# Kernel optimization log

Hardware: AMD Instinct MI355X
Metric: run time of the kernel (lower is better)

The kernel has to match this reference:

```python
import jax, jax.numpy as jnp
import numpy as np


def setup_inputs() -> dict:
    key = jax.random.key(0)
    ks = jax.random.split(key, 8)
    B, S, H = 2, 2048, 2048
    Hq, Hkv, D = 16, 4, H // 16
    s = 0.02
    return {
        "query": jax.random.normal(ks[0], (B, S, H), jnp.float32),
        "key": jax.random.normal(ks[1], (B, S, H), jnp.float32),
        "value": jax.random.normal(ks[2], (B, S, H), jnp.float32),
        "Wq": jax.random.normal(ks[3], (H, Hq * D), jnp.float32) * s,
        "bq": jnp.zeros((Hq * D,), jnp.float32),
        "Wk": jax.random.normal(ks[4], (H, Hkv * D), jnp.float32) * s,
        "bk": jnp.zeros((Hkv * D,), jnp.float32),
        "Wv": jax.random.normal(ks[5], (H, Hkv * D), jnp.float32) * s,
        "bv": jnp.zeros((Hkv * D,), jnp.float32),
        "Wo": jax.random.normal(ks[6], (H, H), jnp.float32) * s,
        "bo": jnp.zeros((H,), jnp.float32),
    }


def reference(query, key, value, Wq, bq, Wk, bk, Wv, bv, Wo, bo):
    Hq, Hkv = 16, 4
    B, S, H = query.shape
    D = H // Hq
    G = Hq // Hkv  # heads per KV group
    # projections
    q = query @ Wq + bq   # [B,S,Hq*D]
    k = key @ Wk + bk     # [B,S,Hkv*D]
    v = value @ Wv + bv   # [B,S,Hkv*D]
    # [B, Hkv(groups), G(heads per group), S, D] for q; [B, Hkv, S, D] for k,v
    q = q.reshape(B, S, Hkv, G, D).transpose(0, 2, 3, 1, 4)
    k = k.reshape(B, S, Hkv, D).transpose(0, 2, 1, 3)
    v = v.reshape(B, S, Hkv, D).transpose(0, 2, 1, 3)
    # NOTE: original module applies NO 1/sqrt(D) scaling -- kept faithful.
    attn = jnp.einsum('bghqd,bgkd->bghqk', q, k)  # [B,Hkv,G,S,S]
    attn = jax.nn.softmax(attn, axis=-1)
    out = jnp.einsum('bghqk,bgkd->bghqd', attn, v)  # [B,Hkv,G,S,D]
    # permute(0,3,1,2,4) -> [B,S,Hkv,G,D] -> [B,S,H]
    out = out.transpose(0, 3, 1, 2, 4).reshape(B, S, H)
    return out @ Wo + bo
```

## Files before the change

### kernel.cpp

```cpp
#include <hip/hip_runtime.h>
#include <hip/hip_bf16.h>
#include <type_traits>
#include <stdint.h>

typedef short bf16x8 __attribute__((ext_vector_type(8)));
typedef short short4v __attribute__((ext_vector_type(4)));
typedef float f32x4 __attribute__((ext_vector_type(4)));
typedef float f32x16 __attribute__((ext_vector_type(16)));

#define GLL16(gp, lp) __builtin_amdgcn_global_load_lds( \
    (const __attribute__((address_space(1))) void*)(gp), \
    (__attribute__((address_space(3))) void*)(lp), 16, 0, 0)

__device__ inline short f2bf(float f) {
    union { float f; uint32_t u; } v;
    v.f = f;
    uint32_t r = (v.u + 0x7FFFu + ((v.u >> 16) & 1u)) >> 16;
    return (short)(uint16_t)r;
}

__device__ inline bf16x8 cvt8(const float4& a, const float4& b) {
    bf16x8 o;
    o[0] = f2bf(a.x); o[1] = f2bf(a.y); o[2] = f2bf(a.z); o[3] = f2bf(a.w);
    o[4] = f2bf(b.x); o[5] = f2bf(b.y); o[6] = f2bf(b.z); o[7] = f2bf(b.w);
    return o;
}

__device__ inline uint32_t cvtpk(float lo, float hi) {
    uint32_t r;
    asm("v_cvt_pk_bf16_f32 %0, %1, %2" : "=v"(r) : "v"(lo), "v"(hi));
    return r;
}

__device__ inline bf16x8 mk8(uint32_t a, uint32_t b, uint32_t c, uint32_t d) {
    union { uint32_t u[4]; bf16x8 v; } t;
    t.u[0] = a; t.u[1] = b; t.u[2] = c; t.u[3] = d;
    return t.v;
}

__device__ inline void xchg_pf(const uint32_t c[8], bool hib, bf16x8& fA, bf16x8& fB) {
    uint32_t p0 = (uint32_t)__shfl_xor((int)c[0], 32);
    uint32_t p1 = (uint32_t)__shfl_xor((int)c[1], 32);
    uint32_t p2 = (uint32_t)__shfl_xor((int)c[2], 32);
    uint32_t p3 = (uint32_t)__shfl_xor((int)c[3], 32);
    fA = mk8(hib ? p2 : c[0], hib ? p3 : c[1], hib ? c[2] : p0, hib ? c[3] : p1);
    uint32_t p4 = (uint32_t)__shfl_xor((int)c[4], 32);
    uint32_t p5 = (uint32_t)__shfl_xor((int)c[5], 32);
    uint32_t p6 = (uint32_t)__shfl_xor((int)c[6], 32);
    uint32_t p7 = (uint32_t)__shfl_xor((int)c[7], 32);
    fB = mk8(hib ? p6 : c[4], hib ? p7 : c[5], hib ? c[6] : p4, hib ? c[7] : p5);
}

__global__ __launch_bounds__(256) void cvtk(const float* __restrict__ in,
                                            short* __restrict__ out, int n8)
{
    int i = blockIdx.x * blockDim.x + threadIdx.x;
    int stride = gridDim.x * blockDim.x;
    for (; i < n8; i += stride) {
        const float4* p = (const float4*)(in + (size_t)i * 8);
        float4 a = p[0], b = p[1];
        *(bf16x8*)(out + (size_t)i * 8) = cvt8(a, b);
    }
}

__global__ __launch_bounds__(256) void cvt3(
    const float* __restrict__ q, const float* __restrict__ k, const float* __restrict__ v,
    short* __restrict__ Xq, short* __restrict__ Xk, short* __restrict__ Xv)
{
    const float* in; short* out;
    if (blockIdx.y == 0) { in = q; out = Xq; }
    else if (blockIdx.y == 1) { in = k; out = Xk; }
    else { in = v; out = Xv; }
    size_t i = (size_t)blockIdx.x * 256 + threadIdx.x;
    const float4* p = (const float4*)(in + i * 8);
    float4 a = p[0], b = p[1];
    *(bf16x8*)(out + i * 8) = cvt8(a, b);
}

__global__ __launch_bounds__(256) void transW4(
    const float* __restrict__ W0, const float* __restrict__ W1,
    const float* __restrict__ W2, const float* __restrict__ W3,
    short* __restrict__ T0, short* __restrict__ T1,
    short* __restrict__ T2, short* __restrict__ T3)
{
    const int K = 2048;
    const float* W; short* T; int N;
    int z = blockIdx.z;
    if (z == 0)      { W = W0; T = T0; N = 2048; }
    else if (z == 1) { W = W1; T = T1; N = 512; }
    else if (z == 2) { W = W2; T = T2; N = 512; }
    else             { W = W3; T = T3; N = 2048; }
    int n0 = blockIdx.x * 64, k0 = blockIdx.y * 64;
    if (n0 >= N) return;
    __shared__ short Tt[64][65];
    int t = threadIdx.x;
    int kl = t >> 2, nb = (t & 3) * 16;
    const float* wp = W + (size_t)(k0 + kl) * N + n0 + nb;
    #pragma unroll
    for (int j = 0; j < 16; ++j) Tt[nb + j][kl] = f2bf(wp[j]);
    __syncthreads();
    int nl = t >> 2, kb = (t & 3) * 16;
    short* op = T + (size_t)(n0 + nl) * K + k0 + kb;
    #pragma unroll
    for (int j = 0; j < 16; ++j) op[j] = Tt[nl][kb + j];
}

__global__ __launch_bounds__(256) void transV(const short* __restrict__ Vb,
                                              short* __restrict__ Vt)
{
    __shared__ short T[64][65];
    int s0 = blockIdx.x * 64, d0 = blockIdx.y * 64, bg = blockIdx.z;
    int b = bg >> 2, g = bg & 3;
    int t = threadIdx.x;
    int sl = t >> 2, db = (t & 3) * 16;
    const short* vp = Vb + (size_t)(b * 2048 + s0 + sl) * 512 + g * 128 + d0 + db;
    #pragma unroll
    for (int j = 0; j < 16; ++j) T[db + j][sl] = vp[j];
    __syncthreads();
    int dl = t >> 2, sb = (t & 3) * 16;
    short* op = Vt + (size_t)(bg * 128 + d0 + dl) * 2048 + s0 + sb;
    #pragma unroll
    for (int j = 0; j < 16; ++j) op[j] = T[dl][sb + j];
}

template <typename TC>
__device__ __forceinline__ void gemm_core(
    const short* __restrict__ A, const short* __restrict__ BT,
    const float* __restrict__ bias, TC* __restrict__ C,
    int N, int K, int m0, int n0, short* As, short* Bs)
{
    const int t = threadIdx.x, w = t >> 6, lane = t & 63;
    const int lr = lane & 15, lg = lane >> 4;
    const int wm = (w >> 1) * 64, wn = (w & 1) * 64;
    f32x4 acc[4][4] = {};

    const int lrow = lane >> 3;
    const int lcg = (lane & 7) ^ (lrow & 7);
    const int sw = lr & 7;

    const short* abase[2]; const short* bbase[2];
    #pragma unroll
    for (int kc = 0; kc < 2; ++kc) {
        abase[kc] = &As[(wm + lr) * 64 + (((kc * 4 + lg) ^ sw) * 8)];
        bbase[kc] = &Bs[(wn + lr) * 64 + (((kc * 4 + lg) ^ sw) * 8)];
    }
    const short* asrc = A  + (size_t)(m0 + w * 32 + lrow) * K + lcg * 8;
    const short* bsrc = BT + (size_t)(n0 + w * 32 + lrow) * K + lcg * 8;
    short* adst = &As[(w * 32) * 64];
    short* bdst = &Bs[(w * 32) * 64];

    for (int kk = 0; kk < K; kk += 64) {
        __syncthreads();
        #pragma unroll
        for (int i = 0; i < 4; ++i) {
            GLL16(asrc + (size_t)i * 8 * K, adst + i * 512);
            GLL16(bsrc + (size_t)i * 8 * K, bdst + i * 512);
        }
        asrc += 64; bsrc += 64;
        __syncthreads();
        #pragma unroll
        for (int kc = 0; kc < 2; ++kc) {
            bf16x8 af[4], bfr[4];
            #pragma unroll
            for (int i = 0; i < 4; ++i) af[i] = *(const bf16x8*)(abase[kc] + i * 1024);
            #pragma unroll
            for (int j = 0; j < 4; ++j) bfr[j] = *(const bf16x8*)(bbase[kc] + j * 1024);
            #pragma unroll
            for (int i = 0; i < 4; ++i)
                #pragma unroll
                for (int j = 0; j < 4; ++j)
                    acc[i][j] = __builtin_amdgcn_mfma_f32_16x16x32_bf16(af[i], bfr[j], acc[i][j], 0, 0, 0);
        }
    }

    #pragma unroll
    for (int i = 0; i < 4; ++i) {
        #pragma unroll
        for (int j = 0; j < 4; ++j) {
            #pragma unroll
            for (int r = 0; r < 4; ++r) {
                int row = m0 + wm + i * 16 + lg * 4 + r;
                int col = n0 + wn + j * 16 + lr;
                float v = acc[i][j][r] + bias[col];
                if constexpr (std::is_same<TC, short>::value)
                    C[(size_t)row * N + col] = f2bf(v);
                else
                    C[(size_t)row * N + col] = v;
            }
        }
    }
}

template <typename TC>
__global__ __launch_bounds__(256) void gemm_std(
    const short* __restrict__ A, const short* __restrict__ BT,
    const float* __restrict__ bias, TC* __restrict__ C, int N, int K)
{
    __shared__ short As[128 * 64];
    __shared__ short Bs[128 * 64];
    int bid = blockIdx.x;
    int chunk = gridDim.x >> 3;
    int wg = (bid & 7) * chunk + (bid >> 3);
    int m0 = (wg & 31) * 128, n0 = (wg >> 5) * 128;
    gemm_core<TC>(A, BT, bias, C, N, K, m0, n0, As, Bs);
}

__global__ __launch_bounds__(256) void gemm_qkv(
    const short* __restrict__ Xq, const short* __restrict__ Xk, const short* __restrict__ Xv,
    const short* __restrict__ WqT, const short* __restrict__ WkT, const short* __restrict__ WvT,
    const float* __restrict__ bq, const float* __restrict__ bk, const float* __restrict__ bv,
    short* __restrict__ Qb, short* __restrict__ Kb, short* __restrict__ Vb)
{
    __shared__ short As[128 * 64];
    __shared__ short Bs[128 * 64];
    int bid = blockIdx.x;
    int wg = (bid & 7) * 96 + (bid >> 3);
    const short* A; const short* BT; const float* bi; short* C; int N; int l;
    if (wg < 512)      { l = wg;       A = Xq; BT = WqT; bi = bq; C = Qb; N = 2048; }
    else if (wg < 640) { l = wg - 512; A = Xk; BT = WkT; bi = bk; C = Kb; N = 512; }
    else               { l = wg - 640; A = Xv; BT = WvT; bi = bv; C = Vb; N = 512; }
    int m0 = (l & 31) * 128, n0 = (l >> 5) * 128;
    gemm_core<short>(A, BT, bi, C, N, 2048, m0, n0, As, Bs);
}

__global__ __launch_bounds__(256, 2) void attn_kernel(
    const short* __restrict__ Qb, const short* __restrict__ Kb,
    const short* __restrict__ Vt, short* __restrict__ Ob)
{
    const int S = 2048;
    __shared__ short Ks[2 * 64 * 128];
    __shared__ short Vs[2 * 128 * 64];

    int bid = blockIdx.x;
    int wg = (bid & 7) * 64 + (bid >> 3);
    const int qt = wg & 15, bh = wg >> 4;
    const int b = bh >> 4, h = bh & 15, g = h >> 2, bg = b * 4 + g;

    const int t = threadIdx.x, w = t >> 6, lane = t & 63;
    const int l5 = lane & 31, hi = lane >> 5;
    const bool hib = hi != 0;
    const int qg = b * S + qt * 128 + w * 32 + l5;
    const float C = 1.44269504089f;

    const short* qrow = Qb + (size_t)qg * 2048 + h * 128 + hi * 8;
    bf16x8 qf[8];
    #pragma unroll
    for (int dm = 0; dm < 8; ++dm)
        qf[dm] = *(const bf16x8*)(qrow + dm * 16);

    f32x16 o[4] = {};
    float m = -1e30f, l = 0.0f;

    const int sr4 = lane >> 4, sc4 = lane & 15;
    const int sr8 = lane >> 3, sc8 = lane & 7;
    const short* ksrc[4]; const short* vsrc[4];
    #pragma unroll
    for (int i = 0; i < 4; ++i) {
        int kr = w * 16 + i * 4 + sr4;
        ksrc[i] = Kb + (size_t)(b * S + kr) * 512 + g * 128 + ((sc4 ^ (kr & 15)) * 8);
        int d = w * 32 + i * 8 + sr8;
        vsrc[i] = Vt + (size_t)(bg * 128 + d) * 2048 + ((sc8 ^ (d & 7)) * 8);
    }

    int kx[8];
    #pragma unroll
    for (int dm = 0; dm < 8; ++dm)
        kx[dm] = (((dm * 2 + hi) ^ (l5 & 15)) * 8);
    int va[4];
    #pragma unroll
    for (int j = 0; j < 4; ++j)
        va[j] = (((2 * j + hi) ^ (l5 & 7)) * 8);

    #define STAGE(BUF, KVI) do { \
        short* kd = Ks + (BUF) * 8192 + (w * 16) * 128; \
        short* vd = Vs + (BUF) * 8192 + (w * 32) * 64; \
        size_t ko = (size_t)(KVI) * 64 * 512; \
        int vo = (KVI) * 64; \
        _Pragma("unroll") \
        for (int i = 0; i < 4; ++i) { \
            GLL16(ksrc[i] + ko, kd + i * 512); \
            GLL16(vsrc[i] + vo, vd + i * 512); \
        } \
    } while (0)

    STAGE(0, 0);
    const int NT = S / 64;
    for (int ti = 0; ti < NT; ++ti) {
        int cur = ti & 1;
        __syncthreads();
        if (ti + 1 < NT) STAGE(cur ^ 1, ti + 1);

        const short* KB = Ks + cur * 8192 + l5 * 128;
        f32x16 p0 = {}, p1 = {};
        #pragma unroll
        for (int dm = 0; dm < 8; ++dm) {
            bf16x8 k0 = *(const bf16x8*)(KB + kx[dm]);
            bf16x8 k1 = *(const bf16x8*)(KB + 4096 + kx[dm]);
            p0 = __builtin_amdgcn_mfma_f32_32x32x16_bf16(k0, qf[dm], p0, 0, 0, 0);
            p1 = __builtin_amdgcn_mfma_f32_32x32x16_bf16(k1, qf[dm], p1, 0, 0, 0);
        }

        float mx = -1e30f;
        #pragma unroll
        for (int e = 0; e < 16; ++e) mx = fmaxf(mx, fmaxf(p0[e], p1[e]));
        mx = fmaxf(mx, __shfl_xor(mx, 32));
        if (__any(mx > m)) {
            float mn = fmaxf(m, mx);
            float sf = exp2f((m - mn) * C);
            m = mn; l *= sf;
            #pragma unroll
            for (int dblk = 0; dblk < 4; ++dblk)
                #pragma unroll
                for (int e = 0; e < 16; ++e) o[dblk][e] *= sf;
        }
        float nmc = -m * C;
        #pragma unroll
        for (int e = 0; e < 16; ++e) {
            p0[e] = exp2f(fmaf(p0[e], C, nmc));
            p1[e] = exp2f(fmaf(p1[e], C, nmc));
        }
        float rs = 0.0f;
        #pragma unroll
        for (int e = 0; e < 16; ++e) rs += p0[e] + p1[e];
        rs += __shfl_xor(rs, 32);
        l += rs;

        uint32_t c0[8], c1[8];
        #pragma unroll
        for (int i = 0; i < 8; ++i) {
            c0[i] = cvtpk(p0[2 * i], p0[2 * i + 1]);
            c1[i] = cvtpk(p1[2 * i], p1[2 * i + 1]);
        }
        bf16x8 pf[4];
        xchg_pf(c0, hib, pf[0], pf[1]);
        xchg_pf(c1, hib, pf[2], pf[3]);

        const short* VB = Vs + cur * 8192 + l5 * 64;
        #pragma unroll
        for (int dblk = 0; dblk < 4; ++dblk) {
            const short* vb = VB + dblk * 2048;
            #pragma unroll
            for (int j = 0; j < 4; ++j) {
                bf16x8 vf = *(const bf16x8*)(vb + va[j]);
                o[dblk] = __builtin_amdgcn_mfma_f32_32x32x16_bf16(vf, pf[j], o[dblk], 0, 0, 0);
            }
        }
    }
    #undef STAGE

    float inv = 1.0f / l;
    short* op = Ob + (size_t)qg * 2048 + h * 128 + hi * 4;
    #pragma unroll
    for (int dblk = 0; dblk < 4; ++dblk) {
        #pragma unroll
        for (int mm = 0; mm < 4; ++mm) {
            short4v s4;
            #pragma unroll
            for (int e = 0; e < 4; ++e) s4[e] = f2bf(o[dblk][mm * 4 + e] * inv);
            *(short4v*)(op + dblk * 32 + mm * 8) = s4;
        }
    }
}

extern "C" void kernel_launch(void* const* d_in, const int* in_sizes, int n_in,
                              void* d_out, int out_size, void* d_ws, size_t ws_size,
                              hipStream_t stream)
{
    const float* query = (const float*)d_in[0];
    const float* key   = (const float*)d_in[1];
    const float* value = (const float*)d_in[2];
    const float* Wq    = (const float*)d_in[3];
    const float* bq    = (const float*)d_in[4];
    const float* Wk    = (const float*)d_in[5];
    const float* bk    = (const float*)d_in[6];
    const float* Wv    = (const float*)d_in[7];
    const float* bv    = (const float*)d_in[8];
    const float* Wo    = (const float*)d_in[9];
    const float* bo    = (const float*)d_in[10];
    float* out = (float*)d_out;

    const int BS = 4096;
    char* ws = (char*)d_ws;
    dim3 blk(256);

    if (ws_size >= (size_t)100663296) {
        short* Xq  = (short*)(ws + 0);
        short* Xk  = (short*)(ws + 16777216);
        short* Xv  = (short*)(ws + 33554432);
        short* Qb  = (short*)(ws + 50331648);
        short* Kb  = (short*)(ws + 67108864);
        short* Vb  = (short*)(ws + 71303168);
        short* Vtg = (short*)(ws + 75497472);
        short* WqT = (short*)(ws + 79691776);
        short* WkT = (short*)(ws + 88080384);
        short* WvT = (short*)(ws + 90177536);
        short* WoT = (short*)(ws + 92274688);
        short* Ob  = Xq;

        transW4<<<dim3(32, 32, 4), blk, 0, stream>>>(Wq, Wk, Wv, Wo, WqT, WkT, WvT, WoT);
        cvt3<<<dim3(4096, 3), blk, 0, stream>>>(query, key, value, Xq, Xk, Xv);
        gemm_qkv<<<768, blk, 0, stream>>>(Xq, Xk, Xv, WqT, WkT, WvT, bq, bk, bv, Qb, Kb, Vb);
        transV<<<dim3(32, 2, 8), blk, 0, stream>>>(Vb, Vtg);
        attn_kernel<<<512, blk, 0, stream>>>(Qb, Kb, Vtg, Ob);
        gemm_std<float><<<512, blk, 0, stream>>>(Ob, WoT, bo, out, 2048, 2048);
    } else {
        short* Qb  = (short*)(ws + 0);
        short* Kb  = (short*)(ws + 16777216);
        short* Vb  = (short*)(ws + 20971520);
        short* Vtg = (short*)(ws + 25165824);
        short* WqT = (short*)(ws + 29360128);
        short* WkT = (short*)(ws + 37748736);
        short* WvT = (short*)(ws + 39845888);
        short* WoT = (short*)(ws + 41943040);
        short* Xbf = (short*)(ws + 50331648);

        transW4<<<dim3(32, 32, 4), blk, 0, stream>>>(Wq, Wk, Wv, Wo, WqT, WkT, WvT, WoT);
        cvtk<<<2048, blk, 0, stream>>>(query, Xbf, BS * 2048 / 8);
        gemm_std<short><<<512, blk, 0, stream>>>(Xbf, WqT, bq, Qb, 2048, 2048);
        cvtk<<<2048, blk, 0, stream>>>(key, Xbf, BS * 2048 / 8);
        gemm_std<short><<<128, blk, 0, stream>>>(Xbf, WkT, bk, Kb, 512, 2048);
        cvtk<<<2048, blk, 0, stream>>>(value, Xbf, BS * 2048 / 8);
        gemm_std<short><<<128, blk, 0, stream>>>(Xbf, WvT, bv, Vb, 512, 2048);
        transV<<<dim3(32, 2, 8), blk, 0, stream>>>(Vb, Vtg);
        attn_kernel<<<512, blk, 0, stream>>>(Qb, Kb, Vtg, Xbf);
        gemm_std<float><<<512, blk, 0, stream>>>(Xbf, WoT, bo, out, 2048, 2048);
    }
}
```

Before: 266.4 us.

## Fuse prep kernels, write V transposed in GEMM epilogue, shrink attention KV tile

Merges the weight transpose and the input bf16 conversion into one prep launch. The V projection GEMM now writes its output directly in the transposed layout the attention kernel reads, which removes the separate transV kernel and its round trip through memory. The attention kernel halves its KV tile from 64 to 32 rows, cutting shared memory per block, and raises the launch-bounds occupancy hint from 2 to 4 blocks. The trade-off is twice as many loop iterations and barriers per block, plus strided short4 stores in the V epilogue.

```diff
diff --git a/kernel.cpp b/kernel.cpp
--- a/kernel.cpp
+++ b/kernel.cpp
@@ -51,6 +51,51 @@
     fB = mk8(hib ? p6 : c[4], hib ? p7 : c[5], hib ? c[6] : p4, hib ? c[7] : p5);
 }
 
+__global__ __launch_bounds__(256) void prep(
+    const float* __restrict__ Wq, const float* __restrict__ Wk,
+    const float* __restrict__ Wv, const float* __restrict__ Wo,
+    short* __restrict__ WqT, short* __restrict__ WkT,
+    short* __restrict__ WvT, short* __restrict__ WoT,
+    const float* __restrict__ q, const float* __restrict__ k, const float* __restrict__ v,
+    short* __restrict__ Xq, short* __restrict__ Xk, short* __restrict__ Xv)
+{
+    __shared__ short Tt[64][65];
+    const int K = 2048;
+    int bid = blockIdx.x;
+    int t = threadIdx.x;
+    if (bid < 2560) {
+        const float* W; short* T; int N; int l;
+        if (bid < 1024)      { W = Wq; T = WqT; N = 2048; l = bid; }
+        else if (bid < 1280) { W = Wk; T = WkT; N = 512;  l = bid - 1024; }
+        else if (bid < 1536) { W = Wv; T = WvT; N = 512;  l = bid - 1280; }
+        else                 { W = Wo; T = WoT; N = 2048; l = bid - 1536; }
+        int nt = N >> 6;
+        int n0 = (l % nt) * 64, k0 = (l / nt) * 64;
+        int kl = t >> 2, nb = (t & 3) * 16;
+        const float* wp = W + (size_t)(k0 + kl) * N + n0 + nb;
+        #pragma unroll
+        for (int j = 0; j < 16; ++j) Tt[nb + j][kl] = f2bf(wp[j]);
+        __syncthreads();
+        int nl = t >> 2, kb = (t & 3) * 16;
+        short* op = T + (size_t)(n0 + nl) * K + k0 + kb;
+        #pragma unroll
+        for (int j = 0; j < 16; ++j) op[j] = Tt[nl][kb + j];
+    } else {
+        size_t tid = (size_t)(bid - 2560) * 256 + t;
+        #pragma unroll
+        for (int it = 0; it < 2; ++it) {
+            size_t i = tid + (size_t)it * 524288;
+            const float4* p;
+            p = (const float4*)(q + i * 8);
+            *(bf16x8*)(Xq + i * 8) = cvt8(p[0], p[1]);
+            p = (const float4*)(k + i * 8);
+            *(bf16x8*)(Xk + i * 8) = cvt8(p[0], p[1]);
+            p = (const float4*)(v + i * 8);
+            *(bf16x8*)(Xv + i * 8) = cvt8(p[0], p[1]);
+        }
+    }
+}
+
 __global__ __launch_bounds__(256) void cvtk(const float* __restrict__ in,
                                             short* __restrict__ out, int n8)
 {
@@ -58,23 +103,8 @@
     int stride = gridDim.x * blockDim.x;
     for (; i < n8; i += stride) {
         const float4* p = (const float4*)(in + (size_t)i * 8);
-        float4 a = p[0], b = p[1];
-        *(bf16x8*)(out + (size_t)i * 8) = cvt8(a, b);
-    }
-}
-
-__global__ __launch_bounds__(256) void cvt3(
-    const float* __restrict__ q, const float* __restrict__ k, const float* __restrict__ v,
-    short* __restrict__ Xq, short* __restrict__ Xk, short* __restrict__ Xv)
-{
-    const float* in; short* out;
-    if (blockIdx.y == 0) { in = q; out = Xq; }
-    else if (blockIdx.y == 1) { in = k; out = Xk; }
-    else { in = v; out = Xv; }
-    size_t i = (size_t)blockIdx.x * 256 + threadIdx.x;
-    const float4* p = (const float4*)(in + i * 8);
-    float4 a = p[0], b = p[1];
-    *(bf16x8*)(out + i * 8) = cvt8(a, b);
+        *(bf16x8*)(out + (size_t)i * 8) = cvt8(p[0], p[1]);
+    }
 }
 
 __global__ __launch_bounds__(256) void transW4(
@@ -127,7 +157,7 @@
 __device__ __forceinline__ void gemm_core(
     const short* __restrict__ A, const short* __restrict__ BT,
     const float* __restrict__ bias, TC* __restrict__ C,
-    int N, int K, int m0, int n0, short* As, short* Bs)
+    int N, int K, int m0, int n0, short* As, short* Bs, int epi)
 {
     const int t = threadIdx.x, w = t >> 6, lane = t & 63;
     const int lr = lane & 15, lg = lane >> 4;
@@ -173,6 +203,24 @@
         }
     }
 
+    if constexpr (std::is_same<TC, short>::value) {
+        if (epi == 1) {
+            #pragma unroll
+            for (int i = 0; i < 4; ++i) {
+                #pragma unroll
+                for (int j = 0; j < 4; ++j) {
+                    int row = m0 + wm + i * 16 + lg * 4;
+                    int col = n0 + wn + j * 16 + lr;
+                    short4v s4;
+                    #pragma unroll
+                    for (int r = 0; r < 4; ++r) s4[r] = f2bf(acc[i][j][r] + bias[col]);
+                    int bb = row >> 11, ss = row & 2047;
+                    *(short4v*)((short*)C + ((size_t)(bb * 4 + (col >> 7)) * 128 + (col & 127)) * 2048 + ss) = s4;
+                }
+            }
+            return;
+        }
+    }
     #pragma unroll
     for (int i = 0; i < 4; ++i) {
         #pragma unroll
@@ -202,34 +250,34 @@
     int chunk = gridDim.x >> 3;
     int wg = (bid & 7) * chunk + (bid >> 3);
     int m0 = (wg & 31) * 128, n0 = (wg >> 5) * 128;
-    gemm_core<TC>(A, BT, bias, C, N, K, m0, n0, As, Bs);
+    gemm_core<TC>(A, BT, bias, C, N, K, m0, n0, As, Bs, 0);
 }
 
 __global__ __launch_bounds__(256) void gemm_qkv(
     const short* __restrict__ Xq, const short* __restrict__ Xk, const short* __restrict__ Xv,
     const short* __restrict__ WqT, const short* __restrict__ WkT, const short* __restrict__ WvT,
     const float* __restrict__ bq, const float* __restrict__ bk, const float* __restrict__ bv,
-    short* __restrict__ Qb, short* __restrict__ Kb, short* __restrict__ Vb)
+    short* __restrict__ Qb, short* __restrict__ Kb, short* __restrict__ Vt)
 {
     __shared__ short As[128 * 64];
     __shared__ short Bs[128 * 64];
     int bid = blockIdx.x;
     int wg = (bid & 7) * 96 + (bid >> 3);
-    const short* A; const short* BT; const float* bi; short* C; int N; int l;
-    if (wg < 512)      { l = wg;       A = Xq; BT = WqT; bi = bq; C = Qb; N = 2048; }
-    else if (wg < 640) { l = wg - 512; A = Xk; BT = WkT; bi = bk; C = Kb; N = 512; }
-    else               { l = wg - 640; A = Xv; BT = WvT; bi = bv; C = Vb; N = 512; }
+    const short* A; const short* BT; const float* bi; short* C; int N; int l; int epi;
+    if (wg < 512)      { l = wg;       A = Xq; BT = WqT; bi = bq; C = Qb; N = 2048; epi = 0; }
+    else if (wg < 640) { l = wg - 512; A = Xk; BT = WkT; bi = bk; C = Kb; N = 512;  epi = 0; }
+    else               { l = wg - 640; A = Xv; BT = WvT; bi = bv; C = Vt; N = 512;  epi = 1; }
     int m0 = (l & 31) * 128, n0 = (l >> 5) * 128;
-    gemm_core<short>(A, BT, bi, C, N, 2048, m0, n0, As, Bs);
-}
-
-__global__ __launch_bounds__(256, 2) void attn_kernel(
+    gemm_core<short>(A, BT, bi, C, N, 2048, m0, n0, As, Bs, epi);
+}
+
+__global__ __launch_bounds__(256, 4) void attn_kernel(
     const short* __restrict__ Qb, const short* __restrict__ Kb,
     const short* __restrict__ Vt, short* __restrict__ Ob)
 {
     const int S = 2048;
-    __shared__ short Ks[2 * 64 * 128];
-    __shared__ short Vs[2 * 128 * 64];
+    __shared__ short Ks[2 * 32 * 128];
+    __shared__ short Vs[2 * 128 * 32];
 
     int bid = blockIdx.x;
     int wg = (bid & 7) * 64 + (bid >> 3);
@@ -252,57 +300,55 @@
     float m = -1e30f, l = 0.0f;
 
     const int sr4 = lane >> 4, sc4 = lane & 15;
-    const int sr8 = lane >> 3, sc8 = lane & 7;
-    const short* ksrc[4]; const short* vsrc[4];
-    #pragma unroll
-    for (int i = 0; i < 4; ++i) {
-        int kr = w * 16 + i * 4 + sr4;
+    const int sr2 = lane >> 2, sc2 = lane & 3;
+    const short* ksrc[2]; const short* vsrc[2];
+    #pragma unroll
+    for (int i = 0; i < 2; ++i) {
+        int kr = w * 8 + i * 4 + sr4;
         ksrc[i] = Kb + (size_t)(b * S + kr) * 512 + g * 128 + ((sc4 ^ (kr & 15)) * 8);
-        int d = w * 32 + i * 8 + sr8;
-        vsrc[i] = Vt + (size_t)(bg * 128 + d) * 2048 + ((sc8 ^ (d & 7)) * 8);
+        int d = w * 32 + i * 16 + sr2;
+        vsrc[i] = Vt + (size_t)(bg * 128 + d) * 2048 + ((sc2 ^ (d & 3)) * 8);
     }
 
     int kx[8];
     #pragma unroll
     for (int dm = 0; dm < 8; ++dm)
         kx[dm] = (((dm * 2 + hi) ^ (l5 & 15)) * 8);
-    int va[4];
-    #pragma unroll
-    for (int j = 0; j < 4; ++j)
-        va[j] = (((2 * j + hi) ^ (l5 & 7)) * 8);
+    int va[2];
+    #pragma unroll
+    for (int j = 0; j < 2; ++j)
+        va[j] = (((2 * j + hi) ^ (l5 & 3)) * 8);
 
     #define STAGE(BUF, KVI) do { \
-        short* kd = Ks + (BUF) * 8192 + (w * 16) * 128; \
-        short* vd = Vs + (BUF) * 8192 + (w * 32) * 64; \
-        size_t ko = (size_t)(KVI) * 64 * 512; \
-        int vo = (KVI) * 64; \
+        short* kd = Ks + (BUF) * 4096 + (w * 8) * 128; \
+        short* vd = Vs + (BUF) * 4096 + (w * 32) * 32; \
+        size_t ko = (size_t)(KVI) * 32 * 512; \
+        int vo = (KVI) * 32; \
         _Pragma("unroll") \
-        for (int i = 0; i < 4; ++i) { \
+        for (int i = 0; i < 2; ++i) { \
             GLL16(ksrc[i] + ko, kd + i * 512); \
             GLL16(vsrc[i] + vo, vd + i * 512); \
         } \
     } while (0)
 
     STAGE(0, 0);
-    const int NT = S / 64;
+    const int NT = S / 32;
     for (int ti = 0; ti < NT; ++ti) {
         int cur = ti & 1;
         __syncthreads();
         if (ti + 1 < NT) STAGE(cur ^ 1, ti + 1);
 
-        const short* KB = Ks + cur * 8192 + l5 * 128;
-        f32x16 p0 = {}, p1 = {};
+        const short* KB = Ks + cur * 4096 + l5 * 128;
+        f32x16 p0 = {};
         #pragma unroll
         for (int dm = 0; dm < 8; ++dm) {
             bf16x8 k0 = *(const bf16x8*)(KB + kx[dm]);
-            bf16x8 k1 = *(const bf16x8*)(KB + 4096 + kx[dm]);
             p0 = __builtin_amdgcn_mfma_f32_32x32x16_bf16(k0, qf[dm], p0, 0, 0, 0);
-            p1 = __builtin_amdgcn_mfma_f32_32x32x16_bf16(k1, qf[dm], p1, 0, 0, 0);
         }
 
         float mx = -1e30f;
         #pragma unroll
-        for (int e = 0; e < 16; ++e) mx = fmaxf(mx, fmaxf(p0[e], p1[e]));
+        for (int e = 0; e < 16; ++e) mx = fmaxf(mx, p0[e]);
         mx = fmaxf(mx, __shfl_xor(mx, 32));
         if (__any(mx > m)) {
             float mn = fmaxf(m, mx);
@@ -315,32 +361,27 @@
         }
         float nmc = -m * C;
         #pragma unroll
-        for (int e = 0; e < 16; ++e) {
+        for (int e = 0; e < 16; ++e)
             p0[e] = exp2f(fmaf(p0[e], C, nmc));
-            p1[e] = exp2f(fmaf(p1[e], C, nmc));
-        }
         float rs = 0.0f;
         #pragma unroll
-        for (int e = 0; e < 16; ++e) rs += p0[e] + p1[e];
+        for (int e = 0; e < 16; ++e) rs += p0[e];
         rs += __shfl_xor(rs, 32);
         l += rs;
 
-        uint32_t c0[8], c1[8];
-        #pragma unroll
-        for (int i = 0; i < 8; ++i) {
+        uint32_t c0[8];
+        #pragma unroll
+        for (int i = 0; i < 8; ++i)
             c0[i] = cvtpk(p0[2 * i], p0[2 * i + 1]);
-            c1[i] = cvtpk(p1[2 * i], p1[2 * i + 1]);
-        }
-        bf16x8 pf[4];
+        bf16x8 pf[2];
         xchg_pf(c0, hib, pf[0], pf[1]);
-        xchg_pf(c1, hib, pf[2], pf[3]);
-
-        const short* VB = Vs + cur * 8192 + l5 * 64;
+
+        const short* VB = Vs + cur * 4096 + l5 * 32;
         #pragma unroll
         for (int dblk = 0; dblk < 4; ++dblk) {
-            const short* vb = VB + dblk * 2048;
-            #pragma unroll
-            for (int j = 0; j < 4; ++j) {
+            const short* vb = VB + dblk * 1024;
+            #pragma unroll
+            for (int j = 0; j < 2; ++j) {
                 bf16x8 vf = *(const bf16x8*)(vb + va[j]);
                 o[dblk] = __builtin_amdgcn_mfma_f32_32x32x16_bf16(vf, pf[j], o[dblk], 0, 0, 0);
             }
@@ -389,7 +430,6 @@
         short* Xv  = (short*)(ws + 33554432);
         short* Qb  = (short*)(ws + 50331648);
         short* Kb  = (short*)(ws + 67108864);
-        short* Vb  = (short*)(ws + 71303168);
         short* Vtg = (short*)(ws + 75497472);
         short* WqT = (short*)(ws + 79691776);
         short* WkT = (short*)(ws + 88080384);
@@ -397,10 +437,9 @@
         short* WoT = (short*)(ws + 92274688);
         short* Ob  = Xq;
 
-        transW4<<<dim3(32, 32, 4), blk, 0, stream>>>(Wq, Wk, Wv, Wo, WqT, WkT, WvT, WoT);
-        cvt3<<<dim3(4096, 3), blk, 0, stream>>>(query, key, value, Xq, Xk, Xv);
-        gemm_qkv<<<768, blk, 0, stream>>>(Xq, Xk, Xv, WqT, WkT, WvT, bq, bk, bv, Qb, Kb, Vb);
-        transV<<<dim3(32, 2, 8), blk, 0, stream>>>(Vb, Vtg);
+        prep<<<4608, blk, 0, stream>>>(Wq, Wk, Wv, Wo, WqT, WkT, WvT, WoT,
+                                       query, key, value, Xq, Xk, Xv);
+        gemm_qkv<<<768, blk, 0, stream>>>(Xq, Xk, Xv, WqT, WkT, WvT, bq, bk, bv, Qb, Kb, Vtg);
         attn_kernel<<<512, blk, 0, stream>>>(Qb, Kb, Vtg, Ob);
         gemm_std<float><<<512, blk, 0, stream>>>(Ob, WoT, bo, out, 2048, 2048);
     } else {
```

Result: slower. 303.0 us (+13.7%).
